# Kernel optimization log

Hardware: AMD Instinct MI355X
Metric: run time of the kernel (lower is better)

The kernel has to match this reference:

```python
import jax, jax.numpy as jnp
import numpy as np

ROPE_BASE = 10000.0

def apply_rope(x):
    # x: (BS, T, H, hd). 1D RoPE over temporal axis with rotate-half convention.
    BS, T, H, hd = x.shape
    half = hd // 2
    inv_freq = 1.0 / (ROPE_BASE ** (jnp.arange(0, half, dtype=jnp.float32) / half))
    angles = jnp.arange(T, dtype=jnp.float32)[:, None] * inv_freq[None, :]  # (T, half)
    cos = jnp.concatenate([jnp.cos(angles), jnp.cos(angles)], axis=-1)[None, :, None, :]  # (1,T,1,hd)
    sin = jnp.concatenate([jnp.sin(angles), jnp.sin(angles)], axis=-1)[None, :, None, :]
    x1, x2 = x[..., :half], x[..., half:]
    x_rot = jnp.concatenate([-x2, x1], axis=-1)
    return (x * cos + x_rot * sin).astype(x.dtype)

def setup_inputs() -> dict:
    key = jax.random.key(0)
    ks = jax.random.split(key, 7)
    B, T_p, T_f, S, d = 4, 8, 8, 256, 512
    v_p = jax.random.normal(ks[0], (B, T_p, S, d), dtype=jnp.float32)
    v_f = jax.random.normal(ks[1], (B, T_f, S, d), dtype=jnp.float32)
    a_p = jax.random.normal(ks[2], (B, T_p, d), dtype=jnp.float32)
    a_f = jax.random.normal(ks[3], (B, T_f, d), dtype=jnp.float32)
    W_qkv = jax.random.normal(ks[4], (d, 3 * d), dtype=jnp.float32) * (d ** -0.5)
    W_proj = jax.random.normal(ks[5], (d, d), dtype=jnp.float32) * (d ** -0.5)
    b_proj = jnp.zeros((d,), dtype=jnp.float32)
    return {"v_p": v_p, "v_f": v_f, "a_p": a_p, "a_f": a_f,
            "W_qkv": W_qkv, "W_proj": W_proj, "b_proj": b_proj}

def reference(v_p, v_f, a_p, a_f, W_qkv, W_proj, b_proj):
    num_heads = 8
    B, T_p, S, d = v_p.shape
    T_f = v_f.shape[1]
    hd = d // num_heads
    scale = hd ** -0.5

    # rearrange 'b t s d -> (b s) t d'
    vp = jnp.transpose(v_p, (0, 2, 1, 3)).reshape(B * S, T_p, d)
    vf = jnp.transpose(v_f, (0, 2, 1, 3)).reshape(B * S, T_f, d)
    # repeat 'b t d -> (b s) t d'
    ap = jnp.broadcast_to(a_p[:, None], (B, S, T_p, d)).reshape(B * S, T_p, d)
    af = jnp.broadcast_to(a_f[:, None], (B, S, T_f, d)).reshape(B * S, T_f, d)

    tokens = jnp.concatenate([vp, vf, ap, af], axis=1)  # (BS, total_T, d)
    BS, total_T = tokens.shape[0], tokens.shape[1]

    qkv = tokens @ W_qkv  # (BS, total_T, 3d), no bias
    q, k, v = jnp.split(qkv, 3, axis=-1)
    q = q.reshape(BS, total_T, num_heads, hd)
    k = k.reshape(BS, total_T, num_heads, hd)
    v = v.reshape(BS, total_T, num_heads, hd)

    q = apply_rope(q)
    k = apply_rope(k)

    # joint bidirectional attention over total_T
    attn = jnp.einsum('bthd,bThd->bhtT', q, k) * scale
    attn = jax.nn.softmax(attn, axis=-1)
    out = jnp.einsum('bhtT,bThd->bthd', attn, v).reshape(BS, total_T, d)

    out = out @ W_proj + b_proj

    vp_o = out[:, :T_p]
    vf_o = out[:, T_p:T_p + T_f]
    ap_o = out[:, T_p + T_f:T_p + T_f + T_p]
    af_o = out[:, T_p + T_f + T_p:]

    # '(b s) t d -> b t s d'
    vp_o = jnp.transpose(vp_o.reshape(B, S, T_p, d), (0, 2, 1, 3))
    vf_o = jnp.transpose(vf_o.reshape(B, S, T_f, d), (0, 2, 1, 3))
    # '(b s) t d -> b s t d' then mean over s
    ap_o = ap_o.reshape(B, S, T_p, d).mean(axis=1)
    af_o = af_o.reshape(B, S, T_f, d).mean(axis=1)
    return (vp_o, vf_o, ap_o, af_o)
```

## Files before the change

kernel.cpp:

```cpp
#include <hip/hip_runtime.h>
#include <math.h>

#define BB   4
#define SS   256
#define DD   512
#define HH   8
#define HD   64
#define HALF 32
#define TT   32
#define TV   16
#define W3   1536
#define MROWS  16448
#define MPAD   16512

#define VP_BASE 0
#define VF_BASE 4194304
#define AP_BASE 8388608
#define AF_BASE 8404992

#define LN10000_OVER_HALF (9.210340371976184f / 32.0f)

typedef _Float16 h2 __attribute__((ext_vector_type(2)));
typedef _Float16 h4 __attribute__((ext_vector_type(4)));
typedef _Float16 h8 __attribute__((ext_vector_type(8)));
typedef float    f4 __attribute__((ext_vector_type(4)));
typedef float    f16v __attribute__((ext_vector_type(16)));

__device__ __forceinline__ float ropefreq(int i) {
    return __expf(-(float)i * LN10000_OVER_HALF);
}

typedef __attribute__((address_space(3))) void*       lds_ptr_t;
typedef const __attribute__((address_space(1))) void* gbl_ptr_t;
__device__ __forceinline__ void async16(const void* g, void* l) {
    __builtin_amdgcn_global_load_lds((gbl_ptr_t)g, (lds_ptr_t)l, 16, 0, 0);
}

__global__ __launch_bounds__(256)
void conv_kernel(const float* __restrict__ v_p, const float* __restrict__ v_f,
                 const float* __restrict__ a_p, const float* __restrict__ a_f,
                 const float* __restrict__ Wqkv, const float* __restrict__ Wp,
                 _Float16* __restrict__ tok, _Float16* __restrict__ Wt,
                 _Float16* __restrict__ Wpt) {
    __shared__ float tile[64 * 65];
    const int bid = blockIdx.x, tid = threadIdx.x;
    if (bid < 8224) {
        int id = bid * 256 + tid;
        int e  = id * 4;
        int r  = e >> 9, c = e & 511;
        const float* src;
        if (r < 16384) {
            int bs = r >> 4, t = r & 15, b = bs >> 8, s = bs & 255;
            src = (t < 8) ? v_p + (size_t)((b * 8 + t) * SS + s) * DD
                          : v_f + (size_t)((b * 8 + t - 8) * SS + s) * DD;
        } else {
            int idx = r - 16384, b = idx >> 4, t2 = idx & 15;
            src = (t2 < 8) ? a_p + (size_t)(b * 8 + t2) * DD
                           : a_f + (size_t)(b * 8 + (t2 - 8)) * DD;
        }
        float4 v = *(const float4*)(src + c);
        h4 o = { (_Float16)v.x, (_Float16)v.y, (_Float16)v.z, (_Float16)v.w };
        *(h4*)(tok + (size_t)r * DD + c) = o;
    } else {
        int tb = bid - 8224;
        const float* src; _Float16* dst; int ld, k0, n0;
        if (tb < 192) {
            src = Wqkv; dst = Wt; ld = W3;
            k0 = (tb & 7) * 64; n0 = (tb >> 3) * 64;
        } else {
            int t2 = tb - 192;
            src = Wp; dst = Wpt; ld = DD;
            k0 = (t2 & 7) * 64; n0 = (t2 >> 3) * 64;
        }
#pragma unroll
        for (int p = 0; p < 16; ++p) {
            int idx = p * 256 + tid, rr = idx >> 6, cc = idx & 63;
            tile[rr * 65 + cc] = src[(size_t)(k0 + rr) * ld + n0 + cc];
        }
        __syncthreads();
#pragma unroll
        for (int p = 0; p < 16; ++p) {
            int idx = p * 256 + tid, rr = idx >> 6, cc = idx & 63;
            dst[(size_t)(n0 + rr) * DD + k0 + cc] = (_Float16)tile[cc * 65 + rr];
        }
    }
}

__global__ __launch_bounds__(256, 3)
void gemm_qkv_kernel(const _Float16* __restrict__ A, const _Float16* __restrict__ Bt,
                     _Float16* __restrict__ C) {
    __shared__ __align__(16) _Float16 As[128 * 64];
    __shared__ __align__(16) _Float16 Bs[128 * 64];
    const int tid = threadIdx.x, lane = tid & 63, wave = tid >> 6;
    const int bid = blockIdx.x;
    const int tm = bid / 12, tn = bid % 12;
    const int m_base = (wave >> 1) * 64, n_base = (wave & 1) * 64;
    const int quad = lane >> 4, l16 = lane & 15;

    f4 acc[4][4] = {};

    int srow[4], soff[4];
#pragma unroll
    for (int p = 0; p < 4; ++p) {
        int ci = p * 256 + tid;
        int r = ci >> 3, sl = ci & 7;
        srow[p] = r;
        soff[p] = (sl ^ (r & 7)) * 8;
    }

    for (int k0 = 0; k0 < 512; k0 += 64) {
#pragma unroll
        for (int p = 0; p < 4; ++p) {
            int ci = p * 256 + tid;
            async16(A  + (size_t)(tm * 128 + srow[p]) * 512 + k0 + soff[p],
                    &As[ci * 8]);
            async16(Bt + (size_t)(tn * 128 + srow[p]) * 512 + k0 + soff[p],
                    &Bs[ci * 8]);
        }
        __syncthreads();

#pragma unroll
        for (int kk = 0; kk < 2; ++kk) {
            h8 af[4], bf[4];
#pragma unroll
            for (int mi = 0; mi < 4; ++mi) {
                int m = m_base + mi * 16 + l16;
                int sl = (kk * 4 + quad) ^ (m & 7);
                af[mi] = *(const h8*)&As[m * 64 + sl * 8];
            }
#pragma unroll
            for (int ni = 0; ni < 4; ++ni) {
                int n = n_base + ni * 16 + l16;
                int sl = (kk * 4 + quad) ^ (n & 7);
                bf[ni] = *(const h8*)&Bs[n * 64 + sl * 8];
            }
#pragma unroll
            for (int mi = 0; mi < 4; ++mi)
#pragma unroll
                for (int ni = 0; ni < 4; ++ni)
                    acc[mi][ni] = __builtin_amdgcn_mfma_f32_16x16x32_f16(
                        af[mi], bf[ni], acc[mi][ni], 0, 0, 0);
        }
        __syncthreads();
    }

#pragma unroll
    for (int mi = 0; mi < 4; ++mi)
#pragma unroll
        for (int ni = 0; ni < 4; ++ni) {
            int row = tm * 128 + m_base + mi * 16 + quad * 4;
            int col = tn * 128 + n_base + ni * 16 + l16;
#pragma unroll
            for (int r = 0; r < 4; ++r)
                C[(size_t)(row + r) * W3 + col] = (_Float16)acc[mi][ni][r];
        }
}

__global__ __launch_bounds__(256)
void attn5_kernel(const _Float16* __restrict__ qkv, _Float16* __restrict__ attnv,
                  _Float16* __restrict__ attna) {
    __shared__ _Float16 VlA[4][32 * 72];
    __shared__ _Float16 PlA[4][32 * 40];
    const int bid = blockIdx.x;
    const int bs = bid >> 1, hh = bid & 1, b = bs >> 8;
    const int tid = threadIdx.x, wave = tid >> 6, lane = tid & 63;
    const int t = lane & 31, half = lane >> 5;
    _Float16* vl = &VlA[wave][0];
    _Float16* pl = &PlA[wave][0];
    const int h = wave + 4 * hh;

    const size_t row = (t < 16) ? (size_t)(bs * 16 + t)
                                : (size_t)(16384 + b * 16 + (t - 16));
    const _Float16* qp = qkv + row * W3 + h * HD;

    float ccA[8], ssA[8], ccB[8], ssB[8];
#pragma unroll
    for (int j = 0; j < 8; ++j) {
        float aA = (float)t * ropefreq(8 * half + j);
        float aB = (float)t * ropefreq(16 + 8 * half + j);
        __sincosf(aA, &ssA[j], &ccA[j]);
        __sincosf(aB, &ssB[j], &ccB[j]);
    }

    h8 v0 = *(const h8*)(qp + 2 * DD + 32 * half);
    h8 v1 = *(const h8*)(qp + 2 * DD + 32 * half + 8);
    h8 v2 = *(const h8*)(qp + 2 * DD + 32 * half + 16);
    h8 v3 = *(const h8*)(qp + 2 * DD + 32 * half + 24);
    *(h8*)&vl[t * 72 + 32 * half +  0] = v0;
    *(h8*)&vl[t * 72 + 32 * half +  8] = v1;
    *(h8*)&vl[t * 72 + 32 * half + 16] = v2;
    *(h8*)&vl[t * 72 + 32 * half + 24] = v3;

    h8 q0 = *(const h8*)(qp + 8 * half);
    h8 q1 = *(const h8*)(qp + 8 * half + 16);
    h8 q2 = *(const h8*)(qp + 8 * half + 32);
    h8 q3 = *(const h8*)(qp + 8 * half + 48);
    h8 k0 = *(const h8*)(qp + DD + 8 * half);
    h8 k1 = *(const h8*)(qp + DD + 8 * half + 16);
    h8 k2 = *(const h8*)(qp + DD + 8 * half + 32);
    h8 k3 = *(const h8*)(qp + DD + 8 * half + 48);

    h8 qf0, qf1, qf2, qf3, kf0, kf1, kf2, kf3;
#pragma unroll
    for (int j = 0; j < 8; ++j) {
        float x1 = (float)q0[j], x2 = (float)q2[j];
        qf0[j] = (_Float16)(0.125f * (x1 * ccA[j] - x2 * ssA[j]));
        qf2[j] = (_Float16)(0.125f * (x2 * ccA[j] + x1 * ssA[j]));
        x1 = (float)q1[j]; x2 = (float)q3[j];
        qf1[j] = (_Float16)(0.125f * (x1 * ccB[j] - x2 * ssB[j]));
        qf3[j] = (_Float16)(0.125f * (x2 * ccB[j] + x1 * ssB[j]));
        x1 = (float)k0[j]; x2 = (float)k2[j];
        kf0[j] = (_Float16)(x1 * ccA[j] - x2 * ssA[j]);
        kf2[j] = (_Float16)(x2 * ccA[j] + x1 * ssA[j]);
        x1 = (float)k1[j]; x2 = (float)k3[j];
        kf1[j] = (_Float16)(x1 * ccB[j] - x2 * ssB[j]);
        kf3[j] = (_Float16)(x2 * ccB[j] + x1 * ssB[j]);
    }

    f16v s = {};
    s = __builtin_amdgcn_mfma_f32_32x32x16_f16(qf0, kf0, s, 0, 0, 0);
    s = __builtin_amdgcn_mfma_f32_32x32x16_f16(qf1, kf1, s, 0, 0, 0);
    s = __builtin_amdgcn_mfma_f32_32x32x16_f16(qf2, kf2, s, 0, 0, 0);
    s = __builtin_amdgcn_mfma_f32_32x32x16_f16(qf3, kf3, s, 0, 0, 0);

#pragma unroll
    for (int r = 0; r < 16; ++r) {
        float m = s[r];
#pragma unroll
        for (int mask = 1; mask <= 16; mask <<= 1)
            m = fmaxf(m, __shfl_xor(m, mask));
        float e = __expf(s[r] - m);
        float sm = e;
#pragma unroll
        for (int mask = 1; mask <= 16; mask <<= 1)
            sm += __shfl_xor(sm, mask);
        float p = e / sm;
        int rr = (r & 3) + 8 * (r >> 2) + 4 * half;
        pl[rr * 40 + t] = (_Float16)p;
    }

    f16v o_acc[2];
#pragma unroll
    for (int n0 = 0; n0 < 2; ++n0) {
        f16v o = {};
#pragma unroll
        for (int kk = 0; kk < 2; ++kk) {
            h8 pf = *(const h8*)&pl[t * 40 + kk * 16 + half * 8];
            h8 vf;
#pragma unroll
            for (int jj = 0; jj < 8; ++jj)
                vf[jj] = vl[(kk * 16 + half * 8 + jj) * 72 + n0 * 32 + t];
            o = __builtin_amdgcn_mfma_f32_32x32x16_f16(pf, vf, o, 0, 0, 0);
        }
        o_acc[n0] = o;
    }

#pragma unroll
    for (int n0 = 0; n0 < 2; ++n0)
#pragma unroll
        for (int r = 0; r < 16; ++r) {
            int i = (r & 3) + 8 * (r >> 2) + 4 * half;
            vl[i * 72 + n0 * 32 + t] = (_Float16)o_acc[n0][r];
        }

#pragma unroll
    for (int rr = 0; rr < 4; ++rr) {
        int i = rr * 8 + (lane >> 3);
        int c = (lane & 7) * 8;
        h8 val = *(const h8*)&vl[i * 72 + c];
        if (rr < 2)
            *(h8*)&attnv[(size_t)(bs * 16 + i) * DD + h * HD + c] = val;
        else
            *(h8*)&attna[((size_t)bs * 16 + (i - 16)) * DD + h * HD + c] = val;
    }
}

__global__ __launch_bounds__(256)
void proj_kernel(const _Float16* __restrict__ A, const _Float16* __restrict__ Bt,
                 const _Float16* __restrict__ attna, const float* __restrict__ Wp,
                 const float* __restrict__ bp, float* __restrict__ out) {
    __shared__ __align__(16) _Float16 As[128 * 32];
    __shared__ __align__(16) _Float16 Bs[64 * 32];
    __shared__ float arow[DD];
    const int bid = blockIdx.x, tid = threadIdx.x;

    if (bid < 1024) {
        const int lane = tid & 63, wave = tid >> 6;
        const int tm = bid >> 3, tn = bid & 7;
        const int m_base = wave * 32;
        const int quad = lane >> 4, l16 = lane & 15;

        f4 acc[2][4] = {};

        for (int k0 = 0; k0 < 512; k0 += 32) {
#pragma unroll
            for (int rnd = 0; rnd < 2; ++rnd) {
                int i = rnd * 256 + tid;
                int r = i >> 2, c = (i & 3) * 8;
                async16(A + (size_t)(tm * 128 + r) * 512 + k0 + c, &As[i * 8]);
            }
            {
                int i = tid;
                int r = i >> 2, c = (i & 3) * 8;
                async16(Bt + (size_t)(tn * 64 + r) * 512 + k0 + c, &Bs[i * 8]);
            }
            __syncthreads();

            h8 af[2], bf[4];
#pragma unroll
            for (int mi = 0; mi < 2; ++mi)
                af[mi] = *(const h8*)&As[(m_base + mi * 16 + l16) * 32 + quad * 8];
#pragma unroll
            for (int ni = 0; ni < 4; ++ni)
                bf[ni] = *(const h8*)&Bs[(ni * 16 + l16) * 32 + quad * 8];
#pragma unroll
            for (int mi = 0; mi < 2; ++mi)
#pragma unroll
                for (int ni = 0; ni < 4; ++ni)
                    acc[mi][ni] = __builtin_amdgcn_mfma_f32_16x16x32_f16(
                        af[mi], bf[ni], acc[mi][ni], 0, 0, 0);
            __syncthreads();
        }

#pragma unroll
        for (int mi = 0; mi < 2; ++mi)
#pragma unroll
            for (int ni = 0; ni < 4; ++ni) {
                int row0 = tm * 128 + m_base + mi * 16 + quad * 4;
                int col  = tn * 64 + ni * 16 + l16;
                float bias = bp[col];
#pragma unroll
                for (int r = 0; r < 4; ++r) {
                    int row = row0 + r;
                    int bsq = row >> 4, t = row & 15;
                    int b = bsq >> 8, s = bsq & 255;
                    size_t off = (t < 8)
                        ? (VP_BASE + (size_t)((b * 8 + t) * SS + s) * DD + col)
                        : (VF_BASE + (size_t)((b * 8 + t - 8) * SS + s) * DD + col);
                    out[off] = acc[mi][ni][r] + bias;
                }
            }
    } else {
        const int r = bid - 1024;
        const int b = r >> 4, t = r & 15;

        float acc0 = 0.f, acc1 = 0.f;
        for (int s = 0; s < SS; ++s) {
            h2 v = *(const h2*)&attna[((size_t)((b * SS + s) * 16 + t)) * DD + tid * 2];
            acc0 += (float)v.x;
            acc1 += (float)v.y;
        }
        arow[tid * 2]     = acc0 * (1.0f / (float)SS);
        arow[tid * 2 + 1] = acc1 * (1.0f / (float)SS);
        __syncthreads();

        for (int jj = 0; jj < 2; ++jj) {
            int j = jj * 256 + tid;
            float acc = bp[j];
            for (int k = 0; k < DD; ++k) acc += arow[k] * Wp[k * DD + j];
            size_t off = (t < 8) ? (AP_BASE + (size_t)(b * 8 + t) * DD + j)
                                 : (AF_BASE + (size_t)(b * 8 + (t - 8)) * DD + j);
            out[off] = acc;
        }
    }
}

extern "C" void kernel_launch(void* const* d_in, const int* in_sizes, int n_in,
                              void* d_out, int out_size, void* d_ws, size_t ws_size,
                              hipStream_t stream) {
    const float* v_p  = (const float*)d_in[0];
    const float* v_f  = (const float*)d_in[1];
    const float* a_p  = (const float*)d_in[2];
    const float* a_f  = (const float*)d_in[3];
    const float* Wqkv = (const float*)d_in[4];
    const float* Wp   = (const float*)d_in[5];
    const float* bp   = (const float*)d_in[6];
    float* out = (float*)d_out;

    char* w = (char*)d_ws;
    _Float16* tok   = (_Float16*)w;  w += (size_t)MPAD * DD * 2;
    _Float16* qkv   = (_Float16*)w;  w += (size_t)MPAD * W3 * 2;
    _Float16* attnv = (_Float16*)w;  w += (size_t)16384 * DD * 2;
    _Float16* Wt    = (_Float16*)w;  w += (size_t)W3 * DD * 2;
    _Float16* Wpt   = (_Float16*)w;  w += (size_t)DD * DD * 2;
    _Float16* attna = tok;

    conv_kernel<<<8480, 256, 0, stream>>>(v_p, v_f, a_p, a_f, Wqkv, Wp,
                                          tok, Wt, Wpt);
    gemm_qkv_kernel<<<129 * 12, 256, 0, stream>>>(tok, Wt, qkv);
    attn5_kernel<<<2048, 256, 0, stream>>>(qkv, attnv, attna);
    proj_kernel<<<1088, 256, 0, stream>>>(attnv, Wpt, attna, Wp, bp, out);
}
```

Baseline: 217.8 us.

## Reduce audio rows before projection and retile proj GEMM with swizzled 128x128 tiles

Audio attention outputs are now written in an s-contiguous layout and averaged over S by a separate reduce kernel. Because the projection is linear, the mean can be taken before it, so the 64 averaged rows are simply appended to the video rows in the projection GEMM. This removes the slow per-block scalar fp32 matvec over Wp from the old proj kernel. The GEMM moves to 128x128 tiles with k=64 steps and XOR-swizzled LDS, and adds a launch-bounds occupancy hint. The cost is an extra kernel launch and averaging in fp16 before the projection rather than after it.

```diff
diff --git a/kernel.cpp b/kernel.cpp
--- a/kernel.cpp
+++ b/kernel.cpp
@@ -162,7 +162,7 @@
     __shared__ _Float16 VlA[4][32 * 72];
     __shared__ _Float16 PlA[4][32 * 40];
     const int bid = blockIdx.x;
-    const int bs = bid >> 1, hh = bid & 1, b = bs >> 8;
+    const int bs = bid >> 1, hh = bid & 1, b = bs >> 8, s = bs & 255;
     const int tid = threadIdx.x, wave = tid >> 6, lane = tid & 63;
     const int t = lane & 31, half = lane >> 5;
     _Float16* vl = &VlA[wave][0];
@@ -217,19 +217,19 @@
         kf3[j] = (_Float16)(x2 * ccB[j] + x1 * ssB[j]);
     }
 
-    f16v s = {};
-    s = __builtin_amdgcn_mfma_f32_32x32x16_f16(qf0, kf0, s, 0, 0, 0);
-    s = __builtin_amdgcn_mfma_f32_32x32x16_f16(qf1, kf1, s, 0, 0, 0);
-    s = __builtin_amdgcn_mfma_f32_32x32x16_f16(qf2, kf2, s, 0, 0, 0);
-    s = __builtin_amdgcn_mfma_f32_32x32x16_f16(qf3, kf3, s, 0, 0, 0);
+    f16v s4 = {};
+    s4 = __builtin_amdgcn_mfma_f32_32x32x16_f16(qf0, kf0, s4, 0, 0, 0);
+    s4 = __builtin_amdgcn_mfma_f32_32x32x16_f16(qf1, kf1, s4, 0, 0, 0);
+    s4 = __builtin_amdgcn_mfma_f32_32x32x16_f16(qf2, kf2, s4, 0, 0, 0);
+    s4 = __builtin_amdgcn_mfma_f32_32x32x16_f16(qf3, kf3, s4, 0, 0, 0);
 
 #pragma unroll
     for (int r = 0; r < 16; ++r) {
-        float m = s[r];
+        float m = s4[r];
 #pragma unroll
         for (int mask = 1; mask <= 16; mask <<= 1)
             m = fmaxf(m, __shfl_xor(m, mask));
-        float e = __expf(s[r] - m);
+        float e = __expf(s4[r] - m);
         float sm = e;
 #pragma unroll
         for (int mask = 1; mask <= 16; mask <<= 1)
@@ -271,98 +271,122 @@
         if (rr < 2)
             *(h8*)&attnv[(size_t)(bs * 16 + i) * DD + h * HD + c] = val;
         else
-            *(h8*)&attna[((size_t)bs * 16 + (i - 16)) * DD + h * HD + c] = val;
+            *(h8*)&attna[(((size_t)b * 16 + (i - 16)) * SS + s) * DD + h * HD + c] = val;
     }
 }
 
 __global__ __launch_bounds__(256)
+void reduce_a_kernel(const _Float16* __restrict__ attna, _Float16* __restrict__ abar) {
+    __shared__ float red[4][DD];
+    const int r = blockIdx.x;
+    const int tid = threadIdx.x;
+    const int sg = tid >> 6, cl = tid & 63;
+
+    float acc[8] = {};
+    const _Float16* base = attna + ((size_t)r * SS + sg * 64) * DD + cl * 8;
+#pragma unroll 4
+    for (int i = 0; i < 64; ++i) {
+        h8 v = *(const h8*)(base + (size_t)i * DD);
+#pragma unroll
+        for (int j = 0; j < 8; ++j) acc[j] += (float)v[j];
+    }
+#pragma unroll
+    for (int j = 0; j < 8; ++j) red[sg][cl * 8 + j] = acc[j];
+    __syncthreads();
+
+    int c = tid * 2;
+    float s0 = red[0][c] + red[1][c] + red[2][c] + red[3][c];
+    float s1 = red[0][c + 1] + red[1][c + 1] + red[2][c + 1] + red[3][c + 1];
+    h2 o = { (_Float16)(s0 * (1.0f / SS)), (_Float16)(s1 * (1.0f / SS)) };
+    *(h2*)&abar[(size_t)r * DD + c] = o;
+}
+
+__global__ __launch_bounds__(256, 3)
 void proj_kernel(const _Float16* __restrict__ A, const _Float16* __restrict__ Bt,
-                 const _Float16* __restrict__ attna, const float* __restrict__ Wp,
                  const float* __restrict__ bp, float* __restrict__ out) {
-    __shared__ __align__(16) _Float16 As[128 * 32];
-    __shared__ __align__(16) _Float16 Bs[64 * 32];
-    __shared__ float arow[DD];
-    const int bid = blockIdx.x, tid = threadIdx.x;
-
-    if (bid < 1024) {
-        const int lane = tid & 63, wave = tid >> 6;
-        const int tm = bid >> 3, tn = bid & 7;
-        const int m_base = wave * 32;
-        const int quad = lane >> 4, l16 = lane & 15;
-
-        f4 acc[2][4] = {};
-
-        for (int k0 = 0; k0 < 512; k0 += 32) {
-#pragma unroll
-            for (int rnd = 0; rnd < 2; ++rnd) {
-                int i = rnd * 256 + tid;
-                int r = i >> 2, c = (i & 3) * 8;
-                async16(A + (size_t)(tm * 128 + r) * 512 + k0 + c, &As[i * 8]);
+    __shared__ __align__(16) _Float16 As[128 * 64];
+    __shared__ __align__(16) _Float16 Bs[128 * 64];
+    const int tid = threadIdx.x, lane = tid & 63, wave = tid >> 6;
+    const int bid = blockIdx.x;
+    const int tm = bid >> 2, tn = bid & 3;
+    const int m_base = (wave >> 1) * 64, n_base = (wave & 1) * 64;
+    const int quad = lane >> 4, l16 = lane & 15;
+
+    f4 acc[4][4] = {};
+
+    int srow[4], soff[4];
+#pragma unroll
+    for (int p = 0; p < 4; ++p) {
+        int ci = p * 256 + tid;
+        int r = ci >> 3, sl = ci & 7;
+        srow[p] = r;
+        soff[p] = (sl ^ (r & 7)) * 8;
+    }
+
+    for (int k0 = 0; k0 < 512; k0 += 64) {
+#pragma unroll
+        for (int p = 0; p < 4; ++p) {
+            int ci = p * 256 + tid;
+            async16(A  + (size_t)(tm * 128 + srow[p]) * 512 + k0 + soff[p],
+                    &As[ci * 8]);
+            async16(Bt + (size_t)(tn * 128 + srow[p]) * 512 + k0 + soff[p],
+                    &Bs[ci * 8]);
+        }
+        __syncthreads();
+
+#pragma unroll
+        for (int kk = 0; kk < 2; ++kk) {
+            h8 af[4], bf[4];
+#pragma unroll
+            for (int mi = 0; mi < 4; ++mi) {
+                int m = m_base + mi * 16 + l16;
+                int sl = (kk * 4 + quad) ^ (m & 7);
+                af[mi] = *(const h8*)&As[m * 64 + sl * 8];
             }
-            {
-                int i = tid;
-                int r = i >> 2, c = (i & 3) * 8;
-                async16(Bt + (size_t)(tn * 64 + r) * 512 + k0 + c, &Bs[i * 8]);
+#pragma unroll
+            for (int ni = 0; ni < 4; ++ni) {
+                int n = n_base + ni * 16 + l16;
+                int sl = (kk * 4 + quad) ^ (n & 7);
+                bf[ni] = *(const h8*)&Bs[n * 64 + sl * 8];
             }
-            __syncthreads();
-
-            h8 af[2], bf[4];
-#pragma unroll
-            for (int mi = 0; mi < 2; ++mi)
-                af[mi] = *(const h8*)&As[(m_base + mi * 16 + l16) * 32 + quad * 8];
-#pragma unroll
-            for (int ni = 0; ni < 4; ++ni)
-                bf[ni] = *(const h8*)&Bs[(ni * 16 + l16) * 32 + quad * 8];
-#pragma unroll
-            for (int mi = 0; mi < 2; ++mi)
+#pragma unroll
+            for (int mi = 0; mi < 4; ++mi)
 #pragma unroll
                 for (int ni = 0; ni < 4; ++ni)
                     acc[mi][ni] = __builtin_amdgcn_mfma_f32_16x16x32_f16(
                         af[mi], bf[ni], acc[mi][ni], 0, 0, 0);
-            __syncthreads();
-        }
-
-#pragma unroll
-        for (int mi = 0; mi < 2; ++mi)
-#pragma unroll
-            for (int ni = 0; ni < 4; ++ni) {
-                int row0 = tm * 128 + m_base + mi * 16 + quad * 4;
-                int col  = tn * 64 + ni * 16 + l16;
-                float bias = bp[col];
-#pragma unroll
-                for (int r = 0; r < 4; ++r) {
-                    int row = row0 + r;
+        }
+        __syncthreads();
+    }
+
+#pragma unroll
+    for (int mi = 0; mi < 4; ++mi)
+#pragma unroll
+        for (int ni = 0; ni < 4; ++ni) {
+            int row0 = tm * 128 + m_base + mi * 16 + quad * 4;
+            int col  = tn * 128 + n_base + ni * 16 + l16;
+            float bias = bp[col];
+#pragma unroll
+            for (int r = 0; r < 4; ++r) {
+                int row = row0 + r;
+                float val = acc[mi][ni][r] + bias;
+                if (row < 16384) {
                     int bsq = row >> 4, t = row & 15;
                     int b = bsq >> 8, s = bsq & 255;
                     size_t off = (t < 8)
                         ? (VP_BASE + (size_t)((b * 8 + t) * SS + s) * DD + col)
                         : (VF_BASE + (size_t)((b * 8 + t - 8) * SS + s) * DD + col);
-                    out[off] = acc[mi][ni][r] + bias;
+                    out[off] = val;
+                } else if (row < 16448) {
+                    int idx = row - 16384;
+                    int b = idx >> 4, t2 = idx & 15;
+                    size_t off = (t2 < 8)
+                        ? (AP_BASE + (size_t)(b * 8 + t2) * DD + col)
+                        : (AF_BASE + (size_t)(b * 8 + (t2 - 8)) * DD + col);
+                    out[off] = val;
                 }
             }
-    } else {
-        const int r = bid - 1024;
-        const int b = r >> 4, t = r & 15;
-
-        float acc0 = 0.f, acc1 = 0.f;
-        for (int s = 0; s < SS; ++s) {
-            h2 v = *(const h2*)&attna[((size_t)((b * SS + s) * 16 + t)) * DD + tid * 2];
-            acc0 += (float)v.x;
-            acc1 += (float)v.y;
-        }
-        arow[tid * 2]     = acc0 * (1.0f / (float)SS);
-        arow[tid * 2 + 1] = acc1 * (1.0f / (float)SS);
-        __syncthreads();
-
-        for (int jj = 0; jj < 2; ++jj) {
-            int j = jj * 256 + tid;
-            float acc = bp[j];
-            for (int k = 0; k < DD; ++k) acc += arow[k] * Wp[k * DD + j];
-            size_t off = (t < 8) ? (AP_BASE + (size_t)(b * 8 + t) * DD + j)
-                                 : (AF_BASE + (size_t)(b * 8 + (t - 8)) * DD + j);
-            out[off] = acc;
-        }
-    }
+        }
 }
 
 extern "C" void kernel_launch(void* const* d_in, const int* in_sizes, int n_in,
@@ -380,14 +404,16 @@
     char* w = (char*)d_ws;
     _Float16* tok   = (_Float16*)w;  w += (size_t)MPAD * DD * 2;
     _Float16* qkv   = (_Float16*)w;  w += (size_t)MPAD * W3 * 2;
-    _Float16* attnv = (_Float16*)w;  w += (size_t)16384 * DD * 2;
+    _Float16* attnv = (_Float16*)w;  w += (size_t)MPAD * DD * 2;
     _Float16* Wt    = (_Float16*)w;  w += (size_t)W3 * DD * 2;
     _Float16* Wpt   = (_Float16*)w;  w += (size_t)DD * DD * 2;
     _Float16* attna = tok;
+    _Float16* abar  = attnv + (size_t)16384 * DD;
 
     conv_kernel<<<8480, 256, 0, stream>>>(v_p, v_f, a_p, a_f, Wqkv, Wp,
                                           tok, Wt, Wpt);
     gemm_qkv_kernel<<<129 * 12, 256, 0, stream>>>(tok, Wt, qkv);
     attn5_kernel<<<2048, 256, 0, stream>>>(qkv, attnv, attna);
-    proj_kernel<<<1088, 256, 0, stream>>>(attnv, Wpt, attna, Wp, bp, out);
-}
+    reduce_a_kernel<<<64, 256, 0, stream>>>(attna, abar);
+    proj_kernel<<<129 * 4, 256, 0, stream>>>(attnv, Wpt, bp, out);
+}
```

Result: faster. 192.8 us (-11.5%).
